# Optimization experiments

Measured on AMD Instinct MI355X. Metric: run time of the kernel, lower is better.

Reference implementation:

```python
import jax, jax.numpy as jnp
import numpy as np

K_NBR = 128        # PyG radius(max_num_neighbors=128)
NEG_FILL = -1e9    # mask value for max-aggregation over invalid neighbors


def fps(pos, m):
    # Farthest point sampling on pos [N,2] -> [m] int32 indices (start at 0).
    n = pos.shape[0]
    def step(carry, _):
        min_d2, last = carry
        d2 = jnp.sum((pos - pos[last]) ** 2, axis=-1)
        min_d2 = jnp.minimum(min_d2, d2)
        nxt = jnp.argmax(min_d2).astype(jnp.int32)
        return (min_d2, nxt), nxt
    init = (jnp.full((n,), 1e10, pos.dtype), jnp.int32(0))
    _, idxs = jax.lax.scan(step, init, None, length=m - 1)
    return jnp.concatenate([jnp.zeros((1,), jnp.int32), idxs])


def set_abstraction(x, pos, ratio, r, W, b):
    # x [B,N,C], pos [B,N,2]. FPS centers, radius neighbors (<=K), PointNetConv
    # message = Linear(cat[x_j, pos_j - pos_i]) (PyG MLP with one layer and
    # plain_last=True is a bare Linear), then max-aggregate per center.
    B, N, C = x.shape
    m = int(N * ratio)
    idx = jax.vmap(lambda p: fps(p, m))(pos)                         # [B,m]
    ctr = jnp.take_along_axis(pos, idx[..., None], axis=1)           # [B,m,2]
    d2 = jnp.sum((ctr[:, :, None, :] - pos[:, None, :, :]) ** 2, -1)  # [B,m,N]
    k = min(K_NBR, N)
    neg_d2, nbr = jax.lax.top_k(-d2, k)                              # [B,m,k]
    valid = (-neg_d2) <= r * r                                       # in-radius mask
    gather = jax.vmap(lambda a, i: a[i])                             # per-sample fancy index
    x_j = gather(x, nbr)                                             # [B,m,k,C]
    rel = gather(pos, nbr) - ctr[:, :, None, :]                      # [B,m,k,2]
    msg = jnp.concatenate([x_j, rel], axis=-1) @ W + b               # [B,m,k,F]
    msg = jnp.where(valid[..., None], msg, NEG_FILL)
    return jnp.max(msg, axis=2), ctr                                 # [B,m,F], [B,m,2]


def encoder(x, zones_ids, lf_W1, lf_b1, lf_W2, lf_b2, c1_W, c1_b, c2_W, c2_b, c3_W, c3_b):
    lf = jnp.tanh(jnp.tanh(x @ lf_W1 + lf_b1) @ lf_W2 + lf_b2)       # [B,N,64]
    h = jnp.concatenate([lf, zones_ids], axis=-1)                    # [B,N,65]
    h, pos = set_abstraction(h, x, 0.5, 0.5, c1_W, c1_b)             # [B,N/2,64]
    h, pos = set_abstraction(h, pos, 0.25, 1.0, c2_W, c2_b)          # [B,N/8,128]
    g = jnp.concatenate([h, pos], axis=-1) @ c3_W + c3_b             # [B,N/8,1024]
    gf = jnp.max(g, axis=1, keepdims=True)                           # global max pool -> [B,1,1024]
    return lf, gf


def setup_inputs():
    key = jax.random.key(0)
    ks = jax.random.split(key, 12)
    B, N = 4, 4096
    def lin(kw, kb, fi, fo):
        return (jax.random.normal(kw, (fi, fo), jnp.float32) / np.sqrt(fi),
                jax.random.normal(kb, (fo,), jnp.float32) * 0.01)
    x = jax.random.normal(ks[0], (B, N, 2), jnp.float32) * 4.0  # spread so ball(r) holds <128 pts
    zones_ids = jax.random.uniform(ks[1], (B, N, 1), jnp.float32)
    lf_W1, lf_b1 = lin(ks[2], ks[3], 2, 64)
    lf_W2, lf_b2 = lin(ks[4], ks[5], 64, 64)
    c1_W, c1_b = lin(ks[6], ks[7], 67, 64)
    c2_W, c2_b = lin(ks[8], ks[9], 66, 128)
    c3_W, c3_b = lin(ks[10], ks[11], 130, 1024)
    return {"x": x, "zones_ids": zones_ids, "lf_W1": lf_W1, "lf_b1": lf_b1,
            "lf_W2": lf_W2, "lf_b2": lf_b2, "c1_W": c1_W, "c1_b": c1_b,
            "c2_W": c2_W, "c2_b": c2_b, "c3_W": c3_W, "c3_b": c3_b}


def reference(x, zones_ids, lf_W1, lf_b1, lf_W2, lf_b2, c1_W, c1_b, c2_W, c2_b, c3_W, c3_b):
    return encoder(x, zones_ids, lf_W1, lf_b1, lf_W2, lf_b2,
                   c1_W, c1_b, c2_W, c2_b, c3_W, c3_b)
```

## Files before the change

### kernel.cpp

```cpp
#include <hip/hip_runtime.h>


constexpr int BB = 4;
constexpr int NN = 4096;
constexpr int M1 = 2048;
constexpr int M2 = 512;

typedef float v2f __attribute__((ext_vector_type(2)));

__device__ __forceinline__ float d2_exact(float dx, float dy) {
    return __fadd_rn(__fmul_rn(dx, dx), __fmul_rn(dy, dy));
}

template<int CTRL>
__device__ __forceinline__ unsigned long long dpp64z(unsigned long long v) {
    unsigned lo = (unsigned)__builtin_amdgcn_update_dpp(0, (int)(unsigned)v, CTRL, 0xF, 0xF, true);
    unsigned hi = (unsigned)__builtin_amdgcn_update_dpp(0, (int)(unsigned)(v >> 32), CTRL, 0xF, 0xF, true);
    return ((unsigned long long)hi << 32) | (unsigned long long)lo;
}
template<int CTRL>
__device__ __forceinline__ void pairc(unsigned long long& t1, unsigned long long& t2) {
    unsigned long long o1 = dpp64z<CTRL>(t1);
    unsigned long long o2 = dpp64z<CTRL>(t2);
    bool g = o1 > t1;
    unsigned long long m1 = g ? o1 : t1;
    unsigned long long sm = g ? t1 : o1;
    unsigned long long cn = g ? o2 : t2;
    t2 = cn > sm ? cn : sm;
    t1 = m1;
}
__device__ __forceinline__ unsigned long long readlane64(unsigned long long v, int l) {
    unsigned lo = (unsigned)__builtin_amdgcn_readlane((int)(unsigned)v, l);
    unsigned hi = (unsigned)__builtin_amdgcn_readlane((int)(unsigned)(v >> 32), l);
    return ((unsigned long long)hi << 32) | (unsigned long long)lo;
}

__global__ __launch_bounds__(256) void k_lf_y1(
    const float2* __restrict__ x, const float* __restrict__ zones,
    const float* __restrict__ W1, const float* __restrict__ b1,
    const float* __restrict__ W2, const float* __restrict__ b2,
    const float* __restrict__ c1W, const float* __restrict__ c1b,
    float* __restrict__ out_lf, float* __restrict__ y1)
{
    __shared__ float sh[4][64];
    __shared__ float sl[4][64];
    int tid = threadIdx.x;
    int p = tid >> 6, f = tid & 63;
    size_t pt = (size_t)blockIdx.x * 4 + p;
    float2 xv = x[pt];
    float hid = tanhf(xv.x * W1[f] + xv.y * W1[64 + f] + b1[f]);
    sh[p][f] = hid;
    __syncthreads();
    float acc = b2[f];
#pragma unroll
    for (int c = 0; c < 64; ++c) acc += sh[p][c] * W2[c * 64 + f];
    float lf = tanhf(acc);
    sl[p][f] = lf;
    out_lf[pt * 64 + f] = lf;
    __syncthreads();
    float acc2 = c1b[f] + zones[pt] * c1W[64 * 64 + f]
               + xv.x * c1W[65 * 64 + f] + xv.y * c1W[66 * 64 + f];
#pragma unroll
    for (int c = 0; c < 64; ++c) acc2 += sl[p][c] * c1W[c * 64 + f];
    y1[pt * 64 + f] = acc2;
}

template<int M, int PPT>
__device__ __forceinline__ void fps_core(
    const float2* __restrict__ src, const float2* __restrict__ PTSl,
    float2* __restrict__ centl, unsigned long long (&slk)[2][8],
    int tid, int lane, int wv)
{
#pragma clang fp contract(off)
    constexpr int PP2 = PPT / 2;
    v2f px2[PP2], py2[PP2], md2[PP2];
#pragma unroll
    for (int k = 0; k < PP2; ++k) {
        float2 a = src[tid + (2 * k) * 256];
        float2 b = src[tid + (2 * k + 1) * 256];
        px2[k] = (v2f){a.x, b.x};
        py2[k] = (v2f){a.y, b.y};
        md2[k] = (v2f){1e10f, 1e10f};
    }
    float2 c0 = src[0];
    if (tid == 0) centl[0] = c0;

    float c1x = c0.x, c1y = c0.y, c2x = 0.0f, c2y = 0.0f;
    bool two = false;
    int it = 1;
    unsigned rc = 0;
    while (it < M) {
        int par = (int)(rc & 1u); ++rc;
        v2f vcx = (v2f){c1x, c1x}, vcy = (v2f){c1y, c1y};
#pragma unroll
        for (int k = 0; k < PP2; ++k) {
            v2f dx = px2[k] - vcx, dy = py2[k] - vcy;
            v2f d2 = (dx * dx) + (dy * dy);
            md2[k] = __builtin_elementwise_min(md2[k], d2);
        }
        if (two) {
            v2f wcx = (v2f){c2x, c2x}, wcy = (v2f){c2y, c2y};
#pragma unroll
            for (int k = 0; k < PP2; ++k) {
                v2f dx = px2[k] - wcx, dy = py2[k] - wcy;
                v2f d2 = (dx * dx) + (dy * dy);
                md2[k] = __builtin_elementwise_min(md2[k], d2);
            }
        }
        unsigned long long t1 = 0ull, t2 = 0ull;
#pragma unroll
        for (int s = 0; s < PPT; ++s) {
            float mq = (s & 1) ? md2[s >> 1].y : md2[s >> 1].x;
            unsigned long long key =
                ((unsigned long long)__float_as_uint(mq) << 32)
                | (unsigned long long)(0xFFFFFFFFu - (unsigned)(tid + s * 256));
            bool g = key > t1;
            unsigned long long ns = g ? t1 : (key > t2 ? key : t2);
            t1 = g ? key : t1;
            t2 = ns;
        }
        pairc<0x111>(t1, t2); pairc<0x112>(t1, t2); pairc<0x114>(t1, t2);
        pairc<0x118>(t1, t2); pairc<0x142>(t1, t2); pairc<0x143>(t1, t2);
        if (lane == 63) { slk[par][2 * wv] = t1; slk[par][2 * wv + 1] = t2; }
        __syncthreads();
        unsigned long long a1 = slk[par][2 * (lane & 3)];
        unsigned long long a2 = slk[par][2 * (lane & 3) + 1];
        if (lane >= 4) { a1 = 0ull; a2 = 0ull; }
        pairc<0x111>(a1, a2); pairc<0x112>(a1, a2);
        unsigned long long w1 = readlane64(a1, 3);
        unsigned long long r1 = readlane64(a2, 3);
        int jw = (int)(0xFFFFFFFFu - (unsigned)w1);
        int jr = (int)(0xFFFFFFFFu - (unsigned)r1);
        float mdr = __uint_as_float((unsigned)(r1 >> 32));
        float2 wpt = PTSl[jw];
        float2 rpt = PTSl[jr];
        float ddx = rpt.x - wpt.x, ddy = rpt.y - wpt.y;
        float dd = (ddx * ddx) + (ddy * ddy);
        bool dbl = (it + 1 < M) && (dd >= mdr);
        if (tid == 0) { centl[it] = wpt; if (dbl) centl[it + 1] = rpt; }
        c1x = wpt.x; c1y = wpt.y; c2x = rpt.x; c2y = rpt.y;
        two = dbl;
        it += dbl ? 2 : 1;
    }
}

__global__ __launch_bounds__(256, 1) void k_fps_fused(
    const float2* __restrict__ pos, float* __restrict__ p1out,
    float* __restrict__ p2out)
{
    __shared__ float2 PTS[NN];
    __shared__ float2 cent1[M1];
    __shared__ float2 cent2[M2];
    __shared__ unsigned long long slk[2][8];
    int tid = threadIdx.x, lane = tid & 63, wv = tid >> 6;
    const float2* p = pos + (size_t)blockIdx.x * NN;

    for (int i = tid; i < NN; i += 256) PTS[i] = p[i];
    __syncthreads();

    fps_core<M1, NN / 256>(p, PTS, cent1, slk, tid, lane, wv);
    __syncthreads();
    float2* o1 = (float2*)(p1out + (size_t)blockIdx.x * M1 * 2);
    for (int i = tid; i < M1; i += 256) o1[i] = cent1[i];

    fps_core<M2, M1 / 256>(cent1, cent1, cent2, slk, tid, lane, wv);
    __syncthreads();
    float2* o2 = (float2*)(p2out + (size_t)blockIdx.x * M2 * 2);
    for (int i = tid; i < M2; i += 256) o2[i] = cent2[i];
}

__global__ __launch_bounds__(256) void k_sa(
    const float2* __restrict__ candpos, const float* __restrict__ y,
    const float* __restrict__ ctr, const float* __restrict__ W,
    int NP, int F, int relrow, float r2, float* __restrict__ hout)
{
    __shared__ int cnt;
    __shared__ int list[4096];
    int tid = threadIdx.x;
    int b = blockIdx.y;
    size_t crow = (size_t)b * gridDim.x + blockIdx.x;
    if (tid == 0) cnt = 0;
    __syncthreads();
    float cx = ctr[crow * 2], cy = ctr[crow * 2 + 1];
    const float2* cp = candpos + (size_t)b * NP;
    for (int j = tid; j < NP; j += 256) {
        float2 pj = cp[j];
        float d2 = d2_exact(pj.x - cx, pj.y - cy);
        if (d2 <= r2) { int t = atomicAdd(&cnt, 1); list[t] = j; }
    }
    __syncthreads();
    int n = cnt;
    for (int f = tid; f < F; f += 256) {
        float m = -3.0e38f;
        for (int t = 0; t < n; ++t)
            m = fmaxf(m, y[((size_t)b * NP + list[t]) * F + f]);
        float ct = cx * W[(size_t)relrow * F + f] + cy * W[(size_t)(relrow + 1) * F + f];
        hout[crow * F + f] = m - ct;
    }
}

__global__ __launch_bounds__(128) void k_y2(
    const float* __restrict__ h1, const float* __restrict__ p1,
    const float* __restrict__ W, const float* __restrict__ bb,
    float* __restrict__ y2)
{
    __shared__ float sh[64];
    size_t row = blockIdx.x;
    int f = threadIdx.x;
    if (f < 64) sh[f] = h1[row * 64 + f];
    __syncthreads();
    float acc = bb[f] + p1[row * 2] * W[64 * 128 + f]
              + p1[row * 2 + 1] * W[65 * 128 + f];
#pragma unroll
    for (int c = 0; c < 64; ++c) acc += sh[c] * W[c * 128 + f];
    y2[row * 128 + f] = acc;
}

__global__ __launch_bounds__(256) void k_g(
    const float* __restrict__ h2, const float* __restrict__ p2,
    const float* __restrict__ W3, const float* __restrict__ b3,
    float* __restrict__ part)
{
    int f = blockIdx.x * 256 + threadIdx.x;
    int b = blockIdx.z;
    int i0 = blockIdx.y * 8;
    float acc[8];
    float bbv = b3[f];
#pragma unroll
    for (int ii = 0; ii < 8; ++ii) acc[ii] = bbv;
    const float* hrow = h2 + ((size_t)b * M2 + i0) * 128;
    for (int c = 0; c < 128; ++c) {
        float w = W3[(size_t)c * 1024 + f];
#pragma unroll
        for (int ii = 0; ii < 8; ++ii) acc[ii] += hrow[ii * 128 + c] * w;
    }
    float wx = W3[(size_t)128 * 1024 + f];
    float wy = W3[(size_t)129 * 1024 + f];
    const float* prow = p2 + ((size_t)b * M2 + i0) * 2;
    float m = -3.0e38f;
#pragma unroll
    for (int ii = 0; ii < 8; ++ii) {
        float g = acc[ii] + prow[ii * 2] * wx + prow[ii * 2 + 1] * wy;
        m = fmaxf(m, g);
    }
    part[((size_t)b * 64 + blockIdx.y) * 1024 + f] = m;
}

__global__ __launch_bounds__(256) void k_gmax(const float* __restrict__ part,
                                              float* __restrict__ outg)
{
    int f = blockIdx.x * 256 + threadIdx.x;
    int b = f >> 10, fl = f & 1023;
    float m = -3.0e38f;
#pragma unroll 8
    for (int ig = 0; ig < 64; ++ig)
        m = fmaxf(m, part[((size_t)b * 64 + ig) * 1024 + fl]);
    outg[f] = m;
}

extern "C" void kernel_launch(void* const* d_in, const int* in_sizes, int n_in,
                              void* d_out, int out_size, void* d_ws, size_t ws_size,
                              hipStream_t stream)
{
    const float* x    = (const float*)d_in[0];
    const float* zon  = (const float*)d_in[1];
    const float* lfW1 = (const float*)d_in[2];
    const float* lfb1 = (const float*)d_in[3];
    const float* lfW2 = (const float*)d_in[4];
    const float* lfb2 = (const float*)d_in[5];
    const float* c1W  = (const float*)d_in[6];
    const float* c1b  = (const float*)d_in[7];
    const float* c2W  = (const float*)d_in[8];
    const float* c2b  = (const float*)d_in[9];
    const float* c3W  = (const float*)d_in[10];
    const float* c3b  = (const float*)d_in[11];
    float* out = (float*)d_out;

    char* w = (char*)d_ws;
    float* big = (float*)w;                    w += (size_t)BB * NN * 64 * 4;
    float* p1  = (float*)w;                    w += (size_t)BB * M1 * 2 * 4;
    float* h1  = (float*)w;                    w += (size_t)BB * M1 * 64 * 4;
    float* p2  = (float*)w;                    w += (size_t)BB * M2 * 2 * 4;
    float* h2  = (float*)w;                    w += (size_t)BB * M2 * 128 * 4;
    float* y1 = big, * y2 = big, * part = big;

    k_lf_y1<<<BB * NN / 4, 256, 0, stream>>>((const float2*)x, zon, lfW1, lfb1,
                                             lfW2, lfb2, c1W, c1b, out, y1);
    k_fps_fused<<<BB, 256, 0, stream>>>((const float2*)x, p1, p2);
    k_sa<<<dim3(M1, BB), 256, 0, stream>>>((const float2*)x, y1, p1, c1W,
                                           NN, 64, 65, 0.25f, h1);
    k_y2<<<BB * M1, 128, 0, stream>>>(h1, p1, c2W, c2b, y2);
    k_sa<<<dim3(M2, BB), 256, 0, stream>>>((const float2*)p1, y2, p2, c2W,
                                           M1, 128, 64, 1.0f, h2);
    k_g<<<dim3(4, 64, BB), 256, 0, stream>>>(h2, p2, c3W, c3b, part);
    k_gmax<<<16, 256, 0, stream>>>(part, out + (size_t)BB * NN * 64);
}
```

Measured before the change: 1.586 ms.

## Replace brute-force FPS with Morton-bucketed chunk pruning in a single wavefront

Farthest point sampling now sorts points into 16-point chunks by a 32x32 Morton grid and keeps a per-chunk bounding box and cached best key. Each round updates only the chunks whose box lies closer to the new center than their current max min-distance, then reduces the per-chunk maxima. All rounds run on one wavefront without block barriers. The goal is to cut both the full N-point distance scan per round and the cross-wave barrier cost. In exchange, the work depends on the data, the divergent ballot loops are serial, three of the four waves sit idle, and the previous two-centers-per-round trick is dropped.

```diff
diff --git a/kernel.cpp b/kernel.cpp
--- a/kernel.cpp
+++ b/kernel.cpp
@@ -5,8 +5,6 @@
 constexpr int NN = 4096;
 constexpr int M1 = 2048;
 constexpr int M2 = 512;
-
-typedef float v2f __attribute__((ext_vector_type(2)));
 
 __device__ __forceinline__ float d2_exact(float dx, float dy) {
     return __fadd_rn(__fmul_rn(dx, dx), __fmul_rn(dy, dy));
@@ -19,20 +17,19 @@
     return ((unsigned long long)hi << 32) | (unsigned long long)lo;
 }
 template<int CTRL>
-__device__ __forceinline__ void pairc(unsigned long long& t1, unsigned long long& t2) {
-    unsigned long long o1 = dpp64z<CTRL>(t1);
-    unsigned long long o2 = dpp64z<CTRL>(t2);
-    bool g = o1 > t1;
-    unsigned long long m1 = g ? o1 : t1;
-    unsigned long long sm = g ? t1 : o1;
-    unsigned long long cn = g ? o2 : t2;
-    t2 = cn > sm ? cn : sm;
-    t1 = m1;
-}
-__device__ __forceinline__ unsigned long long readlane64(unsigned long long v, int l) {
-    unsigned lo = (unsigned)__builtin_amdgcn_readlane((int)(unsigned)v, l);
-    unsigned hi = (unsigned)__builtin_amdgcn_readlane((int)(unsigned)(v >> 32), l);
-    return ((unsigned long long)hi << 32) | (unsigned long long)lo;
+__device__ __forceinline__ float dppfz(float v) {
+    return __uint_as_float((unsigned)__builtin_amdgcn_update_dpp(
+        0, (int)__float_as_uint(v), CTRL, 0xF, 0xF, true));
+}
+template<int CTRL>
+__device__ __forceinline__ void max1p(unsigned long long& k, float& x, float& y) {
+    unsigned long long ok = dpp64z<CTRL>(k);
+    float ox = dppfz<CTRL>(x);
+    float oy = dppfz<CTRL>(y);
+    bool g = ok > k;
+    k = g ? ok : k;
+    x = g ? ox : x;
+    y = g ? oy : y;
 }
 
 __global__ __launch_bounds__(256) void k_lf_y1(
@@ -65,82 +62,176 @@
     y1[pt * 64 + f] = acc2;
 }
 
-template<int M, int PPT>
-__device__ __forceinline__ void fps_core(
-    const float2* __restrict__ src, const float2* __restrict__ PTSl,
-    float2* __restrict__ centl, unsigned long long (&slk)[2][8],
-    int tid, int lane, int wv)
+
+__device__ __forceinline__ unsigned part1by1(unsigned v) {
+    v = (v | (v << 8)) & 0x00FF00FFu;
+    v = (v | (v << 4)) & 0x0F0F0F0Fu;
+    v = (v | (v << 2)) & 0x33333333u;
+    v = (v | (v << 1)) & 0x55555555u;
+    return v;
+}
+__device__ __forceinline__ unsigned mortcid(float px, float py, float lx, float ly,
+                                            float sx, float sy) {
+    int ix = (int)((px - lx) * sx); ix = ix < 0 ? 0 : (ix > 31 ? 31 : ix);
+    int iy = (int)((py - ly) * sy); iy = iy < 0 ? 0 : (iy > 31 ? 31 : iy);
+    return part1by1((unsigned)ix) | (part1by1((unsigned)iy) << 1);
+}
+
+template<int N, int NCg>
+__device__ void build_chunks(const float2* __restrict__ src,
+                             float4* PT, uint4* CB, float4* BBX,
+                             unsigned* HIST, float* red,
+                             int tid, int lane, int wv)
+{
+    float lx = 1e30f, hx = -1e30f, ly = 1e30f, hy = -1e30f;
+    for (int i = tid; i < N; i += 256) {
+        float2 q = src[i];
+        lx = fminf(lx, q.x); hx = fmaxf(hx, q.x);
+        ly = fminf(ly, q.y); hy = fmaxf(hy, q.y);
+    }
+#pragma unroll
+    for (int d = 1; d < 64; d <<= 1) {
+        lx = fminf(lx, __shfl_xor(lx, d)); hx = fmaxf(hx, __shfl_xor(hx, d));
+        ly = fminf(ly, __shfl_xor(ly, d)); hy = fmaxf(hy, __shfl_xor(hy, d));
+    }
+    if (lane == 0) {
+        red[wv * 4 + 0] = lx; red[wv * 4 + 1] = hx;
+        red[wv * 4 + 2] = ly; red[wv * 4 + 3] = hy;
+    }
+    __syncthreads();
+    lx = fminf(fminf(red[0], red[4]),  fminf(red[8],  red[12]));
+    hx = fmaxf(fmaxf(red[1], red[5]),  fmaxf(red[9],  red[13]));
+    ly = fminf(fminf(red[2], red[6]),  fminf(red[10], red[14]));
+    hy = fmaxf(fmaxf(red[3], red[7]),  fmaxf(red[11], red[15]));
+    float sx = 31.999f / fmaxf(hx - lx, 1e-20f);
+    float sy = 31.999f / fmaxf(hy - ly, 1e-20f);
+
+    for (int i = tid; i < 1024; i += 256) HIST[i] = 0u;
+    __syncthreads();
+    for (int i = tid; i < N; i += 256) {
+        float2 q = src[i];
+        atomicAdd(&HIST[mortcid(q.x, q.y, lx, ly, sx, sy)], 1u);
+    }
+    __syncthreads();
+
+    unsigned b0 = HIST[4 * tid], b1 = HIST[4 * tid + 1],
+             b2 = HIST[4 * tid + 2], b3 = HIST[4 * tid + 3];
+    unsigned s = b0 + b1 + b2 + b3;
+    unsigned incl = s;
+#pragma unroll
+    for (int d = 1; d < 64; d <<= 1) {
+        unsigned o = __shfl_up(incl, d);
+        if (lane >= d) incl += o;
+    }
+    if (lane == 63) ((unsigned*)red)[wv] = incl;
+    __syncthreads();
+    unsigned woff = 0;
+    for (int w = 0; w < wv; ++w) woff += ((unsigned*)red)[w];
+    unsigned e = woff + incl - s;
+    HIST[4 * tid]     = e;
+    HIST[4 * tid + 1] = e + b0;
+    HIST[4 * tid + 2] = e + b0 + b1;
+    HIST[4 * tid + 3] = e + b0 + b1 + b2;
+    __syncthreads();
+
+    for (int i = tid; i < N; i += 256) {
+        float2 q = src[i];
+        unsigned slot = atomicAdd(&HIST[mortcid(q.x, q.y, lx, ly, sx, sy)], 1u);
+        PT[slot] = make_float4(q.x, q.y, 1e10f,
+                               __uint_as_float(0xFFFFFFFFu - (unsigned)i));
+    }
+    __syncthreads();
+
+    for (int ci = tid; ci < NCg; ci += 256) {
+        float x0 = 1e30f, x1 = -1e30f, y0 = 1e30f, y1 = -1e30f;
+#pragma unroll
+        for (int j = 0; j < 16; ++j) {
+            float4 q = PT[ci * 16 + j];
+            x0 = fminf(x0, q.x); x1 = fmaxf(x1, q.x);
+            y0 = fminf(y0, q.y); y1 = fmaxf(y1, q.y);
+        }
+        BBX[ci] = make_float4(x0, y0, x1, y1);
+        CB[ci] = make_uint4(0u, 0x7F800000u, 0u, 0u);
+    }
+    __syncthreads();
+}
+
+template<int M, int NCg>
+__device__ void fps_rounds(float4* __restrict__ PT, uint4* __restrict__ CB,
+                           const float4* __restrict__ BBX,
+                           float2* __restrict__ centl, int lane)
 {
 #pragma clang fp contract(off)
-    constexpr int PP2 = PPT / 2;
-    v2f px2[PP2], py2[PP2], md2[PP2];
-#pragma unroll
-    for (int k = 0; k < PP2; ++k) {
-        float2 a = src[tid + (2 * k) * 256];
-        float2 b = src[tid + (2 * k + 1) * 256];
-        px2[k] = (v2f){a.x, b.x};
-        py2[k] = (v2f){a.y, b.y};
-        md2[k] = (v2f){1e10f, 1e10f};
-    }
-    float2 c0 = src[0];
-    if (tid == 0) centl[0] = c0;
-
-    float c1x = c0.x, c1y = c0.y, c2x = 0.0f, c2y = 0.0f;
-    bool two = false;
-    int it = 1;
-    unsigned rc = 0;
-    while (it < M) {
-        int par = (int)(rc & 1u); ++rc;
-        v2f vcx = (v2f){c1x, c1x}, vcy = (v2f){c1y, c1y};
-#pragma unroll
-        for (int k = 0; k < PP2; ++k) {
-            v2f dx = px2[k] - vcx, dy = py2[k] - vcy;
-            v2f d2 = (dx * dx) + (dy * dy);
-            md2[k] = __builtin_elementwise_min(md2[k], d2);
-        }
-        if (two) {
-            v2f wcx = (v2f){c2x, c2x}, wcy = (v2f){c2y, c2y};
-#pragma unroll
-            for (int k = 0; k < PP2; ++k) {
-                v2f dx = px2[k] - wcx, dy = py2[k] - wcy;
-                v2f d2 = (dx * dx) + (dy * dy);
-                md2[k] = __builtin_elementwise_min(md2[k], d2);
+    constexpr int K = NCg / 64;
+    float4 bb[K];
+    uint4 cbc[K];
+#pragma unroll
+    for (int k = 0; k < K; ++k) {
+        bb[k] = BBX[k * 64 + lane];
+        cbc[k] = make_uint4(0u, 0x7F800000u, 0u, 0u);
+    }
+    float2 c0 = centl[0];
+    float cx = c0.x, cy = c0.y;
+    int g4 = lane >> 4, l16 = lane & 15;
+
+    for (int it = 1; it < M; ++it) {
+#pragma unroll
+        for (int k = 0; k < K; ++k) {
+            float bmd = __uint_as_float(cbc[k].y);
+            float dx = fmaxf(fmaxf(bb[k].x - cx, cx - bb[k].z), 0.0f);
+            float dy = fmaxf(fmaxf(bb[k].y - cy, cy - bb[k].w), 0.0f);
+            float bd2 = d2_exact(dx, dy);
+            unsigned long long mk = __ballot(bd2 < bmd);
+            while (mk) {
+                int n0 = (int)__builtin_ctzll(mk); mk &= mk - 1;
+                int n1 = 64, n2 = 64, n3 = 64;
+                if (mk) { n1 = (int)__builtin_ctzll(mk); mk &= mk - 1;
+                  if (mk) { n2 = (int)__builtin_ctzll(mk); mk &= mk - 1;
+                    if (mk) { n3 = (int)__builtin_ctzll(mk); mk &= mk - 1; } } }
+                int nb = g4 == 0 ? n0 : (g4 == 1 ? n1 : (g4 == 2 ? n2 : n3));
+                if (nb < 64) {
+                    int cid = k * 64 + nb;
+                    int base = cid * 16 + l16;
+                    float4 q = PT[base];
+                    float d2 = d2_exact(q.x - cx, q.y - cy);
+                    float nmd = fminf(q.z, d2);
+                    PT[base].z = nmd;
+                    unsigned long long key =
+                        ((unsigned long long)__float_as_uint(nmd) << 32)
+                        | (unsigned long long)__float_as_uint(q.w);
+                    float px = q.x, py = q.y;
+                    max1p<0x111>(key, px, py);
+                    max1p<0x112>(key, px, py);
+                    max1p<0x114>(key, px, py);
+                    max1p<0x118>(key, px, py);
+                    if (l16 == 15)
+                        CB[cid] = make_uint4((unsigned)key, (unsigned)(key >> 32),
+                                             __float_as_uint(px), __float_as_uint(py));
+                }
             }
         }
-        unsigned long long t1 = 0ull, t2 = 0ull;
-#pragma unroll
-        for (int s = 0; s < PPT; ++s) {
-            float mq = (s & 1) ? md2[s >> 1].y : md2[s >> 1].x;
-            unsigned long long key =
-                ((unsigned long long)__float_as_uint(mq) << 32)
-                | (unsigned long long)(0xFFFFFFFFu - (unsigned)(tid + s * 256));
-            bool g = key > t1;
-            unsigned long long ns = g ? t1 : (key > t2 ? key : t2);
-            t1 = g ? key : t1;
-            t2 = ns;
+        unsigned long long bk = 0ull;
+        float bx = 0.0f, by = 0.0f;
+#pragma unroll
+        for (int k = 0; k < K; ++k) {
+            uint4 cb = CB[k * 64 + lane];
+            cbc[k] = cb;
+            unsigned long long kk =
+                ((unsigned long long)cb.y << 32) | (unsigned long long)cb.x;
+            bool gg = kk > bk;
+            bk = gg ? kk : bk;
+            bx = gg ? __uint_as_float(cb.z) : bx;
+            by = gg ? __uint_as_float(cb.w) : by;
         }
-        pairc<0x111>(t1, t2); pairc<0x112>(t1, t2); pairc<0x114>(t1, t2);
-        pairc<0x118>(t1, t2); pairc<0x142>(t1, t2); pairc<0x143>(t1, t2);
-        if (lane == 63) { slk[par][2 * wv] = t1; slk[par][2 * wv + 1] = t2; }
-        __syncthreads();
-        unsigned long long a1 = slk[par][2 * (lane & 3)];
-        unsigned long long a2 = slk[par][2 * (lane & 3) + 1];
-        if (lane >= 4) { a1 = 0ull; a2 = 0ull; }
-        pairc<0x111>(a1, a2); pairc<0x112>(a1, a2);
-        unsigned long long w1 = readlane64(a1, 3);
-        unsigned long long r1 = readlane64(a2, 3);
-        int jw = (int)(0xFFFFFFFFu - (unsigned)w1);
-        int jr = (int)(0xFFFFFFFFu - (unsigned)r1);
-        float mdr = __uint_as_float((unsigned)(r1 >> 32));
-        float2 wpt = PTSl[jw];
-        float2 rpt = PTSl[jr];
-        float ddx = rpt.x - wpt.x, ddy = rpt.y - wpt.y;
-        float dd = (ddx * ddx) + (ddy * ddy);
-        bool dbl = (it + 1 < M) && (dd >= mdr);
-        if (tid == 0) { centl[it] = wpt; if (dbl) centl[it + 1] = rpt; }
-        c1x = wpt.x; c1y = wpt.y; c2x = rpt.x; c2y = rpt.y;
-        two = dbl;
-        it += dbl ? 2 : 1;
+        max1p<0x111>(bk, bx, by); max1p<0x112>(bk, bx, by);
+        max1p<0x114>(bk, bx, by); max1p<0x118>(bk, bx, by);
+        max1p<0x142>(bk, bx, by); max1p<0x143>(bk, bx, by);
+        float wx = __uint_as_float((unsigned)__builtin_amdgcn_readlane(
+                       (int)__float_as_uint(bx), 63));
+        float wy = __uint_as_float((unsigned)__builtin_amdgcn_readlane(
+                       (int)__float_as_uint(by), 63));
+        if (lane == 0) centl[it] = make_float2(wx, wy);
+        cx = wx; cy = wy;
     }
 }
 
@@ -148,25 +239,31 @@
     const float2* __restrict__ pos, float* __restrict__ p1out,
     float* __restrict__ p2out)
 {
-    __shared__ float2 PTS[NN];
-    __shared__ float2 cent1[M1];
-    __shared__ float2 cent2[M2];
-    __shared__ unsigned long long slk[2][8];
+    __shared__ float4 PT[NN];
+    __shared__ uint4  CB[NN / 16];
+    __shared__ float4 BBX[NN / 16];
+    __shared__ unsigned HIST[1024];
+    __shared__ float2 C1[M1];
+    __shared__ float2 C2[M2];
+    __shared__ float red[16];
     int tid = threadIdx.x, lane = tid & 63, wv = tid >> 6;
     const float2* p = pos + (size_t)blockIdx.x * NN;
 
-    for (int i = tid; i < NN; i += 256) PTS[i] = p[i];
-    __syncthreads();
-
-    fps_core<M1, NN / 256>(p, PTS, cent1, slk, tid, lane, wv);
+    build_chunks<NN, NN / 16>(p, PT, CB, BBX, HIST, red, tid, lane, wv);
+    if (tid == 0) C1[0] = p[0];
+    __syncthreads();
+    if (wv == 0) fps_rounds<M1, NN / 16>(PT, CB, BBX, C1, lane);
     __syncthreads();
     float2* o1 = (float2*)(p1out + (size_t)blockIdx.x * M1 * 2);
-    for (int i = tid; i < M1; i += 256) o1[i] = cent1[i];
-
-    fps_core<M2, M1 / 256>(cent1, cent1, cent2, slk, tid, lane, wv);
+    for (int i = tid; i < M1; i += 256) o1[i] = C1[i];
+
+    build_chunks<M1, M1 / 16>((const float2*)C1, PT, CB, BBX, HIST, red, tid, lane, wv);
+    if (tid == 0) C2[0] = C1[0];
+    __syncthreads();
+    if (wv == 0) fps_rounds<M2, M1 / 16>(PT, CB, BBX, C2, lane);
     __syncthreads();
     float2* o2 = (float2*)(p2out + (size_t)blockIdx.x * M2 * 2);
-    for (int i = tid; i < M2; i += 256) o2[i] = cent2[i];
+    for (int i = tid; i < M2; i += 256) o2[i] = C2[i];
 }
 
 __global__ __launch_bounds__(256) void k_sa(
```

New measurement: 2.606 ms. +64.2%, slower.

## Carry candidate coordinates through FPS argmax reduction instead of LDS lookup

Applied to the files above, without the earlier changes.

The FPS argmax reduction now carries the x/y coordinates of the top-two candidates alongside their keys through the DPP lane reductions and the cross-wave shared-memory exchange. The winner's position is read directly via readlane, so the shared-memory point copy (PTS) and the dependent LDS lookups after each reduction are removed. The intent is to shorten the serial per-iteration critical path of FPS and free LDS. In exchange it adds extra DPP moves and selects per reduction step, plus a register-select tree to pick the lane's candidate point.

```diff
diff --git a/kernel.cpp b/kernel.cpp
--- a/kernel.cpp
+++ b/kernel.cpp
@@ -19,20 +19,53 @@
     return ((unsigned long long)hi << 32) | (unsigned long long)lo;
 }
 template<int CTRL>
-__device__ __forceinline__ void pairc(unsigned long long& t1, unsigned long long& t2) {
+__device__ __forceinline__ float dppfz(float v) {
+    return __uint_as_float((unsigned)__builtin_amdgcn_update_dpp(
+        0, (int)__float_as_uint(v), CTRL, 0xF, 0xF, true));
+}
+__device__ __forceinline__ float readlanef(float v, int l) {
+    return __uint_as_float((unsigned)__builtin_amdgcn_readlane((int)__float_as_uint(v), l));
+}
+
+template<int CTRL>
+__device__ __forceinline__ void pairp(unsigned long long& t1, float& x1, float& y1,
+                                      unsigned long long& t2, float& x2, float& y2) {
     unsigned long long o1 = dpp64z<CTRL>(t1);
     unsigned long long o2 = dpp64z<CTRL>(t2);
+    float ox1 = dppfz<CTRL>(x1), oy1 = dppfz<CTRL>(y1);
+    float ox2 = dppfz<CTRL>(x2), oy2 = dppfz<CTRL>(y2);
     bool g = o1 > t1;
     unsigned long long m1 = g ? o1 : t1;
+    float mx = g ? ox1 : x1, my = g ? oy1 : y1;
     unsigned long long sm = g ? t1 : o1;
+    float sx = g ? x1 : ox1, sy = g ? y1 : oy1;
     unsigned long long cn = g ? o2 : t2;
-    t2 = cn > sm ? cn : sm;
-    t1 = m1;
-}
-__device__ __forceinline__ unsigned long long readlane64(unsigned long long v, int l) {
-    unsigned lo = (unsigned)__builtin_amdgcn_readlane((int)(unsigned)v, l);
-    unsigned hi = (unsigned)__builtin_amdgcn_readlane((int)(unsigned)(v >> 32), l);
-    return ((unsigned long long)hi << 32) | (unsigned long long)lo;
+    float nx = g ? ox2 : x2, ny = g ? oy2 : y2;
+    bool h = cn > sm;
+    t2 = h ? cn : sm; x2 = h ? nx : sx; y2 = h ? ny : sy;
+    t1 = m1; x1 = mx; y1 = my;
+}
+
+template<int PP2>
+__device__ __forceinline__ void sel_pt(const v2f (&px2)[PP2], const v2f (&py2)[PP2],
+                                       unsigned s, float& X, float& Y) {
+    unsigned k = s >> 1;
+    v2f vx, vy;
+    if constexpr (PP2 == 8) {
+        v2f x0 = (k & 1) ? px2[1] : px2[0], x1 = (k & 1) ? px2[3] : px2[2];
+        v2f x2 = (k & 1) ? px2[5] : px2[4], x3 = (k & 1) ? px2[7] : px2[6];
+        v2f y0 = (k & 1) ? py2[1] : py2[0], y1 = (k & 1) ? py2[3] : py2[2];
+        v2f y2 = (k & 1) ? py2[5] : py2[4], y3 = (k & 1) ? py2[7] : py2[6];
+        v2f xa = (k & 2) ? x1 : x0, xb = (k & 2) ? x3 : x2;
+        v2f ya = (k & 2) ? y1 : y0, yb = (k & 2) ? y3 : y2;
+        vx = (k & 4) ? xb : xa; vy = (k & 4) ? yb : ya;
+    } else {
+        v2f x0 = (k & 1) ? px2[1] : px2[0], x1 = (k & 1) ? px2[3] : px2[2];
+        v2f y0 = (k & 1) ? py2[1] : py2[0], y1 = (k & 1) ? py2[3] : py2[2];
+        vx = (k & 2) ? x1 : x0; vy = (k & 2) ? y1 : y0;
+    }
+    X = (s & 1) ? vx.y : vx.x;
+    Y = (s & 1) ? vy.y : vy.x;
 }
 
 __global__ __launch_bounds__(256) void k_lf_y1(
@@ -67,9 +100,8 @@
 
 template<int M, int PPT>
 __device__ __forceinline__ void fps_core(
-    const float2* __restrict__ src, const float2* __restrict__ PTSl,
-    float2* __restrict__ centl, unsigned long long (&slk)[2][8],
-    int tid, int lane, int wv)
+    const float2* __restrict__ src, float2* __restrict__ centl,
+    uint4 (&slk)[2][4][2], int tid, int lane, int wv)
 {
 #pragma clang fp contract(off)
     constexpr int PP2 = PPT / 2;
@@ -119,26 +151,44 @@
             t1 = g ? key : t1;
             t2 = ns;
         }
-        pairc<0x111>(t1, t2); pairc<0x112>(t1, t2); pairc<0x114>(t1, t2);
-        pairc<0x118>(t1, t2); pairc<0x142>(t1, t2); pairc<0x143>(t1, t2);
-        if (lane == 63) { slk[par][2 * wv] = t1; slk[par][2 * wv + 1] = t2; }
+        float x1p, y1p, x2p, y2p;
+        unsigned base = 0xFFFFFFFFu - (unsigned)tid;
+        sel_pt<PP2>(px2, py2, (base - (unsigned)t1) >> 8, x1p, y1p);
+        sel_pt<PP2>(px2, py2, (base - (unsigned)t2) >> 8, x2p, y2p);
+        pairp<0x111>(t1, x1p, y1p, t2, x2p, y2p);
+        pairp<0x112>(t1, x1p, y1p, t2, x2p, y2p);
+        pairp<0x114>(t1, x1p, y1p, t2, x2p, y2p);
+        pairp<0x118>(t1, x1p, y1p, t2, x2p, y2p);
+        pairp<0x142>(t1, x1p, y1p, t2, x2p, y2p);
+        pairp<0x143>(t1, x1p, y1p, t2, x2p, y2p);
+        if (lane == 63) {
+            slk[par][wv][0] = make_uint4((unsigned)t1, (unsigned)(t1 >> 32),
+                                         __float_as_uint(x1p), __float_as_uint(y1p));
+            slk[par][wv][1] = make_uint4((unsigned)t2, (unsigned)(t2 >> 32),
+                                         __float_as_uint(x2p), __float_as_uint(y2p));
+        }
         __syncthreads();
-        unsigned long long a1 = slk[par][2 * (lane & 3)];
-        unsigned long long a2 = slk[par][2 * (lane & 3) + 1];
+        uint4 e1 = slk[par][lane & 3][0];
+        uint4 e2 = slk[par][lane & 3][1];
+        unsigned long long a1 = ((unsigned long long)e1.y << 32) | (unsigned long long)e1.x;
+        unsigned long long a2 = ((unsigned long long)e2.y << 32) | (unsigned long long)e2.x;
+        float ax1 = __uint_as_float(e1.z), ay1 = __uint_as_float(e1.w);
+        float ax2 = __uint_as_float(e2.z), ay2 = __uint_as_float(e2.w);
         if (lane >= 4) { a1 = 0ull; a2 = 0ull; }
-        pairc<0x111>(a1, a2); pairc<0x112>(a1, a2);
-        unsigned long long w1 = readlane64(a1, 3);
-        unsigned long long r1 = readlane64(a2, 3);
-        int jw = (int)(0xFFFFFFFFu - (unsigned)w1);
-        int jr = (int)(0xFFFFFFFFu - (unsigned)r1);
-        float mdr = __uint_as_float((unsigned)(r1 >> 32));
-        float2 wpt = PTSl[jw];
-        float2 rpt = PTSl[jr];
-        float ddx = rpt.x - wpt.x, ddy = rpt.y - wpt.y;
+        pairp<0x111>(a1, ax1, ay1, a2, ax2, ay2);
+        pairp<0x112>(a1, ax1, ay1, a2, ax2, ay2);
+        unsigned mdr_u = (unsigned)__builtin_amdgcn_readlane((int)(unsigned)(a2 >> 32), 3);
+        float wx = readlanef(ax1, 3), wy = readlanef(ay1, 3);
+        float rx = readlanef(ax2, 3), ry = readlanef(ay2, 3);
+        float mdr = __uint_as_float(mdr_u);
+        float ddx = rx - wx, ddy = ry - wy;
         float dd = (ddx * ddx) + (ddy * ddy);
         bool dbl = (it + 1 < M) && (dd >= mdr);
-        if (tid == 0) { centl[it] = wpt; if (dbl) centl[it + 1] = rpt; }
-        c1x = wpt.x; c1y = wpt.y; c2x = rpt.x; c2y = rpt.y;
+        if (tid == 0) {
+            centl[it] = make_float2(wx, wy);
+            if (dbl) centl[it + 1] = make_float2(rx, ry);
+        }
+        c1x = wx; c1y = wy; c2x = rx; c2y = ry;
         two = dbl;
         it += dbl ? 2 : 1;
     }
@@ -148,22 +198,18 @@
     const float2* __restrict__ pos, float* __restrict__ p1out,
     float* __restrict__ p2out)
 {
-    __shared__ float2 PTS[NN];
     __shared__ float2 cent1[M1];
     __shared__ float2 cent2[M2];
-    __shared__ unsigned long long slk[2][8];
+    __shared__ uint4 slk[2][4][2];
     int tid = threadIdx.x, lane = tid & 63, wv = tid >> 6;
     const float2* p = pos + (size_t)blockIdx.x * NN;
 
-    for (int i = tid; i < NN; i += 256) PTS[i] = p[i];
-    __syncthreads();
-
-    fps_core<M1, NN / 256>(p, PTS, cent1, slk, tid, lane, wv);
+    fps_core<M1, NN / 256>(p, cent1, slk, tid, lane, wv);
     __syncthreads();
     float2* o1 = (float2*)(p1out + (size_t)blockIdx.x * M1 * 2);
     for (int i = tid; i < M1; i += 256) o1[i] = cent1[i];
 
-    fps_core<M2, M1 / 256>(cent1, cent1, cent2, slk, tid, lane, wv);
+    fps_core<M2, M1 / 256>(cent1, cent2, slk, tid, lane, wv);
     __syncthreads();
     float2* o2 = (float2*)(p2out + (size_t)blockIdx.x * M2 * 2);
     for (int i = tid; i < M2; i += 256) o2[i] = cent2[i];
```

Measured after the change: 2.238 ms. +41.0%, slower.
